# Kernel optimization log

Hardware: AMD Instinct MI355X
Metric: run time of the kernel (lower is better)

The kernel has to match this reference:

```python
import jax, jax.numpy as jnp
import numpy as np

DIM = 512
HIDDEN = DIM * 4


def _act_quant(x):
    # per-token int8 absmax quant over last axis (BitNet b1.58)
    scale = 127.0 / jnp.clip(jnp.max(jnp.abs(x), axis=-1, keepdims=True), 1e-5)
    return jnp.clip(jnp.round(x * scale), -128.0, 127.0) / scale


def _weight_quant(w):
    # ternary {-1,0,1} quant with global mean-abs scale
    scale = 1.0 / jnp.clip(jnp.mean(jnp.abs(w)), 1e-5)
    return jnp.clip(jnp.round(w * scale), -1.0, 1.0) / scale


def _bitlinear(x, w, b):
    # straight-through estimator: forward uses quantized values
    xq = x + jax.lax.stop_gradient(_act_quant(x) - x)
    wq = w + jax.lax.stop_gradient(_weight_quant(w) - w)
    return jnp.einsum('btd,hd->bth', xq, wq) + b


def setup_inputs() -> dict:
    key = jax.random.key(0)
    k1, k2, k3 = jax.random.split(key, 3)
    x = jax.random.normal(k1, (8, 8192, DIM), dtype=jnp.float32)
    w1 = jax.random.normal(k2, (HIDDEN, DIM), dtype=jnp.float32) * (DIM ** -0.5)
    b1 = jnp.zeros((HIDDEN,), dtype=jnp.float32)
    w2 = jax.random.normal(k3, (DIM, HIDDEN), dtype=jnp.float32) * (HIDDEN ** -0.5)
    b2 = jnp.zeros((DIM,), dtype=jnp.float32)
    return {"x": x, "w1": w1, "b1": b1, "w2": w2, "b2": b2}


def reference(x, w1, b1, w2, b2):
    h = _bitlinear(x, w1, b1)                      # [B,T,HIDDEN]
    h = jax.nn.gelu(h, approximate=False)          # exact erf GELU (nn.GELU default)
    return x + _bitlinear(h, w2, b2)               # residual
```

## Files before the change

### kernel.cpp

```cpp
#include <hip/hip_runtime.h>
#include <hip/hip_bf16.h>

#define DIM 512
#define HID 2048
#define MT  64
#define KS1 8
#define KS2 32

typedef __attribute__((ext_vector_type(4))) int      i32x4;
typedef __attribute__((ext_vector_type(4))) unsigned u32x4;

static __device__ __forceinline__ float gelu_erf(float h) {
  const float u  = h * 0.70710678118654752f;
  const float au = fabsf(u);
  const float t  = __builtin_amdgcn_rcpf(fmaf(0.3275911f, au, 1.f));
  float p = fmaf(1.061405429f, t, -1.453152027f);
  p = fmaf(p, t, 1.421413741f);
  p = fmaf(p, t, -0.284496736f);
  p = fmaf(p, t, 0.254829592f);
  p *= t;
  const float e  = __builtin_amdgcn_exp2f(-u * u * 1.4426950408889634f);
  const float ea = fmaf(-p, e, 1.f);
  const float er = __builtin_copysignf(ea, u);
  return fmaf(0.5f * h, er, 0.5f * h);
}

static __device__ __forceinline__ int qi8(float g, float s) {
  return (int)fminf(fmaxf(rintf(g * s), -128.f), 127.f);
}

static __device__ __forceinline__ unsigned q4pack(float4 v, float scl) {
  int q0 = qi8(v.x, scl), q1 = qi8(v.y, scl), q2 = qi8(v.z, scl), q3 = qi8(v.w, scl);
  return (unsigned)(q0 & 255) | ((unsigned)(q1 & 255) << 8) |
         ((unsigned)(q2 & 255) << 16) | ((unsigned)(q3 & 255) << 24);
}

__global__ void k_wabs(const float* __restrict__ w1, const float* __restrict__ w2,
                       float* __restrict__ part) {
  const int b = blockIdx.x;
  const float* src = (b < 256 ? w1 : w2) + (size_t)(b & 255) * 4096 + threadIdx.x * 16;
  float s = 0.f;
#pragma unroll
  for (int i = 0; i < 4; ++i) {
    float4 v = *(const float4*)(src + i * 4);
    s += fabsf(v.x) + fabsf(v.y) + fabsf(v.z) + fabsf(v.w);
  }
  __shared__ float red[256];
  red[threadIdx.x] = s;
  __syncthreads();
  for (int off = 128; off > 0; off >>= 1) {
    if (threadIdx.x < (unsigned)off) red[threadIdx.x] += red[threadIdx.x + off];
    __syncthreads();
  }
  if (threadIdx.x == 0) part[b] = red[0];
}

__global__ void k_wscale(const float* __restrict__ part, float* __restrict__ scales) {
  __shared__ float s1[256], s2[256];
  s1[threadIdx.x] = part[threadIdx.x];
  s2[threadIdx.x] = part[256 + threadIdx.x];
  __syncthreads();
  for (int off = 128; off > 0; off >>= 1) {
    if (threadIdx.x < (unsigned)off) {
      s1[threadIdx.x] += s1[threadIdx.x + off];
      s2[threadIdx.x] += s2[threadIdx.x + off];
    }
    __syncthreads();
  }
  if (threadIdx.x == 0) {
    const float mc1 = fmaxf(s1[0] / 1048576.f, 1e-5f);
    const float mc2 = fmaxf(s2[0] / 1048576.f, 1e-5f);
    scales[0] = mc1; scales[1] = 1.f / mc1;
    scales[2] = mc2; scales[3] = 1.f / mc2;
  }
}

__global__ void k_pack(const float* __restrict__ w1, const float* __restrict__ w2,
                       const float* __restrict__ scales,
                       signed char* __restrict__ p1, signed char* __restrict__ p2) {
  int slot = blockIdx.x * 256 + threadIdx.x;
  const bool isw2 = slot >= 65536;
  const float* w = isw2 ? w2 : w1;
  const float scl = isw2 ? scales[3] : scales[1];
  signed char* p = isw2 ? p2 : p1;
  const int K  = isw2 ? HID : DIM;
  const int KS = isw2 ? KS2 : KS1;
  slot &= 65535;
  const int lane = slot & 63;
  const int fr   = slot >> 6;
  const int nt   = fr / KS;
  const int ks   = fr - nt * KS;
  const int n  = nt * 16 + (lane & 15);
  const int k0 = ks * 64 + (lane >> 4) * 16;
  const float* src = w + (size_t)n * K + k0;
  i32x4 outv;
#pragma unroll
  for (int d = 0; d < 4; ++d) {
    unsigned v = 0;
#pragma unroll
    for (int e = 0; e < 4; ++e) {
      int q = (int)fminf(fmaxf(rintf(src[d * 4 + e] * scl), -1.f), 1.f);
      v |= ((unsigned)(q & 255)) << (8 * e);
    }
    outv[d] = (int)v;
  }
  *(i32x4*)(p + (size_t)slot * 16) = outv;
}

__global__ __launch_bounds__(1024, 4) void k_fused(
    const float* __restrict__ x, const float* __restrict__ b1,
    const float* __restrict__ b2, const signed char* __restrict__ p1,
    const signed char* __restrict__ p2, const float* __restrict__ scales,
    float* __restrict__ out) {
  __shared__ __align__(16) signed char qh[131072];
  __shared__ __align__(16) signed char xq[32768];

  float* rxTab = (float*)qh;
  float* scrP  = (float*)(qh + 1024);
  float* scrQ  = (float*)(qh + 5120);
  float* scrS  = (float*)(qh + 9216);

  const int tid = threadIdx.x;
  const int wv = tid >> 6, ln = tid & 63, lg = ln >> 4, lr = ln & 15;
  const int tok0 = blockIdx.x * MT;
  const float wsc1 = scales[0], wsc2 = scales[2];
  const int swz = (lr & 7) << 4;

  {
    const int row = tid >> 4, sub = tid & 15;
    const float4* xr = (const float4*)(x + (size_t)(tok0 + row) * DIM);
    float4 v[8];
    float am = 0.f;
#pragma unroll
    for (int i = 0; i < 8; ++i) {
      v[i] = xr[i * 16 + sub];
      am = fmaxf(am, fmaxf(fmaxf(fabsf(v[i].x), fabsf(v[i].y)),
                           fmaxf(fabsf(v[i].z), fabsf(v[i].w))));
    }
#pragma unroll
    for (int m = 1; m < 16; m <<= 1) am = fmaxf(am, __shfl_xor(am, m));
    const float mc  = fmaxf(am, 1e-5f);
    const float scl = 127.f / mc;
    if (sub == 0) rxTab[row] = mc * (1.f / 127.f) * wsc1;
    const int rswz = (row & 7) << 4;
#pragma unroll
    for (int i = 0; i < 8; ++i) {
      const unsigned u = q4pack(v[i], scl);
      const int k = i * 64 + sub * 4;
      *(unsigned*)&xq[row * DIM + (((k & ~15) ^ rswz) | (k & 15))] = u;
    }
  }
  __syncthreads();

  float rxw[4];
#pragma unroll
  for (int mt = 0; mt < 4; ++mt) rxw[mt] = rxTab[mt * 16 + lr];

  float hvmax[4], hvmin[4];
#pragma unroll
  for (int mt = 0; mt < 4; ++mt) { hvmax[mt] = -3.4e38f; hvmin[mt] = 3.4e38f; }

#pragma unroll 1
  for (int ch = 0; ch < 4; ++ch) {
    i32x4 acc[2][4];
#pragma unroll
    for (int t = 0; t < 2; ++t)
#pragma unroll
      for (int mt = 0; mt < 4; ++mt) acc[t][mt] = (i32x4){0, 0, 0, 0};
#pragma unroll 2
    for (int ks = 0; ks < KS1; ++ks) {
      i32x4 a[4];
#pragma unroll
      for (int mt = 0; mt < 4; ++mt)
        a[mt] = *(const i32x4*)&xq[(mt * 16 + lr) * DIM + ((ks * 64 + lg * 16) ^ swz)];
#pragma unroll
      for (int t = 0; t < 2; ++t) {
        const int ntg = wv * 8 + ch * 2 + t;
        const i32x4 bfr = *(const i32x4*)(p1 + ((size_t)(ntg * KS1 + ks) * 64 + ln) * 16);
#pragma unroll
        for (int mt = 0; mt < 4; ++mt)
          acc[t][mt] = __builtin_amdgcn_mfma_i32_16x16x64_i8(bfr, a[mt], acc[t][mt], 0, 0, 0);
      }
    }
#pragma unroll
    for (int t = 0; t < 2; ++t) {
      const int ntg = wv * 8 + ch * 2 + t;
      const float4 b4 = *(const float4*)&b1[ntg * 16 + lg * 4];
#pragma unroll
      for (int mt = 0; mt < 4; ++mt) {
#pragma unroll
        for (int r = 0; r < 4; ++r) {
          const float bias = r == 0 ? b4.x : r == 1 ? b4.y : r == 2 ? b4.z : b4.w;
          const float hv = fmaf((float)acc[t][mt][r], rxw[mt], bias);
          hvmax[mt] = fmaxf(hvmax[mt], hv);
          hvmin[mt] = fminf(hvmin[mt], hv);
        }
      }
    }
  }

#pragma unroll
  for (int mt = 0; mt < 4; ++mt) {
    hvmax[mt] = fmaxf(hvmax[mt], __shfl_xor(hvmax[mt], 16));
    hvmax[mt] = fmaxf(hvmax[mt], __shfl_xor(hvmax[mt], 32));
    hvmin[mt] = fminf(hvmin[mt], __shfl_xor(hvmin[mt], 16));
    hvmin[mt] = fminf(hvmin[mt], __shfl_xor(hvmin[mt], 32));
  }
  if (ln < 16) {
#pragma unroll
    for (int mt = 0; mt < 4; ++mt) {
      scrP[wv * 64 + mt * 16 + lr] = hvmax[mt];
      scrQ[wv * 64 + mt * 16 + lr] = hvmin[mt];
    }
  }
  __syncthreads();
  if (tid < MT) {
    float hx = scrP[tid], hn = scrQ[tid];
#pragma unroll
    for (int w = 1; w < 16; ++w) {
      hx = fmaxf(hx, scrP[w * 64 + tid]);
      hn = fminf(hn, scrQ[w * 64 + tid]);
    }
    const float posg = gelu_erf(hx);
    const float negg = (hn <= -0.7518f) ? 0.1699705f : fabsf(gelu_erf(hn));
    const float mg = fmaxf(fmaxf(posg, negg), 1e-5f);
    scrS[tid] = 127.f / mg;
  }
  __syncthreads();

  float s2w[4];
#pragma unroll
  for (int mt = 0; mt < 4; ++mt) s2w[mt] = scrS[mt * 16 + lr];
  __syncthreads();

#pragma unroll 1
  for (int ch = 0; ch < 4; ++ch) {
    i32x4 acc[2][4];
#pragma unroll
    for (int t = 0; t < 2; ++t)
#pragma unroll
      for (int mt = 0; mt < 4; ++mt) acc[t][mt] = (i32x4){0, 0, 0, 0};
#pragma unroll 2
    for (int ks = 0; ks < KS1; ++ks) {
      i32x4 a[4];
#pragma unroll
      for (int mt = 0; mt < 4; ++mt)
        a[mt] = *(const i32x4*)&xq[(mt * 16 + lr) * DIM + ((ks * 64 + lg * 16) ^ swz)];
#pragma unroll
      for (int t = 0; t < 2; ++t) {
        const int ntg = wv * 8 + ch * 2 + t;
        const i32x4 bfr = *(const i32x4*)(p1 + ((size_t)(ntg * KS1 + ks) * 64 + ln) * 16);
#pragma unroll
        for (int mt = 0; mt < 4; ++mt)
          acc[t][mt] = __builtin_amdgcn_mfma_i32_16x16x64_i8(bfr, a[mt], acc[t][mt], 0, 0, 0);
      }
    }
#pragma unroll
    for (int t = 0; t < 2; ++t) {
      const int ntg = wv * 8 + ch * 2 + t;
      const float4 b4 = *(const float4*)&b1[ntg * 16 + lg * 4];
#pragma unroll
      for (int mt = 0; mt < 4; ++mt) {
        const int m = mt * 16 + lr;
        unsigned pk = 0;
#pragma unroll
        for (int r = 0; r < 4; ++r) {
          const float bias = r == 0 ? b4.x : r == 1 ? b4.y : r == 2 ? b4.z : b4.w;
          const float hv = fmaf((float)acc[t][mt][r], rxw[mt], bias);
          const float g  = gelu_erf(hv);
          pk |= ((unsigned)(qi8(g, s2w[mt]) & 255)) << (8 * r);
        }
        *(unsigned*)&qh[m * HID + (((ntg * 16) ^ ((m & 7) << 4)) + lg * 4)] = pk;
      }
    }
  }
  __syncthreads();

  i32x4 acc2[2][4];
#pragma unroll
  for (int t = 0; t < 2; ++t)
#pragma unroll
    for (int mt = 0; mt < 4; ++mt) acc2[t][mt] = (i32x4){0, 0, 0, 0};
#pragma unroll 2
  for (int ks = 0; ks < KS2; ++ks) {
    i32x4 a[4];
#pragma unroll
    for (int mt = 0; mt < 4; ++mt)
      a[mt] = *(const i32x4*)&qh[(mt * 16 + lr) * HID + ((ks * 64 + lg * 16) ^ swz)];
#pragma unroll
    for (int t = 0; t < 2; ++t) {
      const int nt = wv * 2 + t;
      const i32x4 bfr = *(const i32x4*)(p2 + ((size_t)(nt * KS2 + ks) * 64 + ln) * 16);
#pragma unroll
      for (int mt = 0; mt < 4; ++mt)
        acc2[t][mt] = __builtin_amdgcn_mfma_i32_16x16x64_i8(bfr, a[mt], acc2[t][mt], 0, 0, 0);
    }
  }
#pragma unroll
  for (int t = 0; t < 2; ++t) {
    const int n0 = (wv * 2 + t) * 16 + lg * 4;
    const float4 b4 = *(const float4*)&b2[n0];
#pragma unroll
    for (int mt = 0; mt < 4; ++mt) {
      const int m = mt * 16 + lr;
      const float r2 = wsc2 * __builtin_amdgcn_rcpf(s2w[mt]);
      const size_t gbase = (size_t)(tok0 + m) * DIM + n0;
      const float4 x4 = *(const float4*)&x[gbase];
      float4 o;
      o.x = fmaf((float)acc2[t][mt][0], r2, b4.x + x4.x);
      o.y = fmaf((float)acc2[t][mt][1], r2, b4.y + x4.y);
      o.z = fmaf((float)acc2[t][mt][2], r2, b4.z + x4.z);
      o.w = fmaf((float)acc2[t][mt][3], r2, b4.w + x4.w);
      *(float4*)&out[gbase] = o;
    }
  }
}

extern "C" void kernel_launch(void* const* d_in, const int* in_sizes, int n_in,
                              void* d_out, int out_size, void* d_ws, size_t ws_size,
                              hipStream_t stream) {
  const float* x  = (const float*)d_in[0];
  const float* w1 = (const float*)d_in[1];
  const float* b1 = (const float*)d_in[2];
  const float* w2 = (const float*)d_in[3];
  const float* b2 = (const float*)d_in[4];
  float* out = (float*)d_out;

  float* wpart   = (float*)d_ws;
  float* wscales = wpart + 512;
  signed char* p1 = (signed char*)((char*)d_ws + 4096);
  signed char* p2 = (signed char*)((char*)d_ws + 4096 + 1048576);

  k_wabs<<<512, 256, 0, stream>>>(w1, w2, wpart);
  k_wscale<<<1, 256, 0, stream>>>(wpart, wscales);
  k_pack<<<512, 256, 0, stream>>>(w1, w2, wscales, p1, p2);
  k_fused<<<1024, 1024, 0, stream>>>(x, b1, b2, p1, p2, wscales, out);
}
```

Baseline: 291.7 us.

## Compute first GEMM once, cache GELU outputs as fp16 in registers

Removes the second pass of the first int8 GEMM by computing GELU once, taking the exact per-token absmax, and holding the GELU values as packed fp16 in registers until the quantization scale is known. Token tile per block is halved to 32, shrinking shared memory and doubling the grid so more blocks can be resident. The trade-off is more register pressure, halved reuse of weight fragments per block, and fp16 round-toward-zero storage that can occasionally shift an int8 rounding decision.

```diff
diff --git a/kernel.cpp b/kernel.cpp
--- a/kernel.cpp
+++ b/kernel.cpp
@@ -3,12 +3,13 @@
 
 #define DIM 512
 #define HID 2048
-#define MT  64
+#define MT  32
 #define KS1 8
 #define KS2 32
 
 typedef __attribute__((ext_vector_type(4))) int      i32x4;
 typedef __attribute__((ext_vector_type(4))) unsigned u32x4;
+typedef __attribute__((ext_vector_type(2))) __fp16   fp16x2;
 
 static __device__ __forceinline__ float gelu_erf(float h) {
   const float u  = h * 0.70710678118654752f;
@@ -33,6 +34,16 @@
   int q0 = qi8(v.x, scl), q1 = qi8(v.y, scl), q2 = qi8(v.z, scl), q3 = qi8(v.w, scl);
   return (unsigned)(q0 & 255) | ((unsigned)(q1 & 255) << 8) |
          ((unsigned)(q2 & 255) << 16) | ((unsigned)(q3 & 255) << 24);
+}
+
+static __device__ __forceinline__ unsigned packf16(float a, float b) {
+  fp16x2 v = __builtin_amdgcn_cvt_pkrtz(a, b);
+  unsigned u; __builtin_memcpy(&u, &v, 4); return u;
+}
+static __device__ __forceinline__ float unpackf16(unsigned u, int hi) {
+  unsigned short s = (unsigned short)(hi ? (u >> 16) : (u & 0xffff));
+  __fp16 h; __builtin_memcpy(&h, &s, 2);
+  return (float)h;
 }
 
 __global__ void k_wabs(const float* __restrict__ w1, const float* __restrict__ w2,
@@ -112,13 +123,12 @@
     const float* __restrict__ b2, const signed char* __restrict__ p1,
     const signed char* __restrict__ p2, const float* __restrict__ scales,
     float* __restrict__ out) {
-  __shared__ __align__(16) signed char qh[131072];
-  __shared__ __align__(16) signed char xq[32768];
+  __shared__ __align__(16) signed char qh[MT * HID];
+  __shared__ __align__(16) signed char xq[MT * DIM];
 
   float* rxTab = (float*)qh;
   float* scrP  = (float*)(qh + 1024);
-  float* scrQ  = (float*)(qh + 5120);
-  float* scrS  = (float*)(qh + 9216);
+  float* scrS  = (float*)(qh + 4096);
 
   const int tid = threadIdx.x;
   const int wv = tid >> 6, ln = tid & 63, lg = ln >> 4, lr = ln & 15;
@@ -127,172 +137,152 @@
   const int swz = (lr & 7) << 4;
 
   {
-    const int row = tid >> 4, sub = tid & 15;
+    const int row = tid >> 5, sub = tid & 31;
     const float4* xr = (const float4*)(x + (size_t)(tok0 + row) * DIM);
-    float4 v[8];
+    float4 v[4];
     float am = 0.f;
 #pragma unroll
-    for (int i = 0; i < 8; ++i) {
-      v[i] = xr[i * 16 + sub];
+    for (int i = 0; i < 4; ++i) {
+      v[i] = xr[i * 32 + sub];
       am = fmaxf(am, fmaxf(fmaxf(fabsf(v[i].x), fabsf(v[i].y)),
                            fmaxf(fabsf(v[i].z), fabsf(v[i].w))));
     }
 #pragma unroll
-    for (int m = 1; m < 16; m <<= 1) am = fmaxf(am, __shfl_xor(am, m));
+    for (int m = 1; m < 32; m <<= 1) am = fmaxf(am, __shfl_xor(am, m));
     const float mc  = fmaxf(am, 1e-5f);
     const float scl = 127.f / mc;
     if (sub == 0) rxTab[row] = mc * (1.f / 127.f) * wsc1;
     const int rswz = (row & 7) << 4;
 #pragma unroll
-    for (int i = 0; i < 8; ++i) {
+    for (int i = 0; i < 4; ++i) {
       const unsigned u = q4pack(v[i], scl);
-      const int k = i * 64 + sub * 4;
-      *(unsigned*)&xq[row * DIM + (((k & ~15) ^ rswz) | (k & 15))] = u;
-    }
-  }
-  __syncthreads();
-
-  float rxw[4];
-#pragma unroll
-  for (int mt = 0; mt < 4; ++mt) rxw[mt] = rxTab[mt * 16 + lr];
-
-  float hvmax[4], hvmin[4];
-#pragma unroll
-  for (int mt = 0; mt < 4; ++mt) { hvmax[mt] = -3.4e38f; hvmin[mt] = 3.4e38f; }
-
-#pragma unroll 1
-  for (int ch = 0; ch < 4; ++ch) {
-    i32x4 acc[2][4];
-#pragma unroll
-    for (int t = 0; t < 2; ++t)
-#pragma unroll
-      for (int mt = 0; mt < 4; ++mt) acc[t][mt] = (i32x4){0, 0, 0, 0};
-#pragma unroll 2
-    for (int ks = 0; ks < KS1; ++ks) {
-      i32x4 a[4];
-#pragma unroll
-      for (int mt = 0; mt < 4; ++mt)
-        a[mt] = *(const i32x4*)&xq[(mt * 16 + lr) * DIM + ((ks * 64 + lg * 16) ^ swz)];
-#pragma unroll
-      for (int t = 0; t < 2; ++t) {
-        const int ntg = wv * 8 + ch * 2 + t;
-        const i32x4 bfr = *(const i32x4*)(p1 + ((size_t)(ntg * KS1 + ks) * 64 + ln) * 16);
-#pragma unroll
-        for (int mt = 0; mt < 4; ++mt)
-          acc[t][mt] = __builtin_amdgcn_mfma_i32_16x16x64_i8(bfr, a[mt], acc[t][mt], 0, 0, 0);
-      }
-    }
+      const int c = (i * 32 + sub) * 4;
+      *(unsigned*)&xq[row * DIM + (((c & ~15) ^ rswz) | (c & 15))] = u;
+    }
+  }
+  __syncthreads();
+
+  float rxw[2];
+#pragma unroll
+  for (int mt = 0; mt < 2; ++mt) rxw[mt] = rxTab[mt * 16 + lr];
+
+  unsigned gpk[4][2][2][2];
+  float gmax[2] = {0.f, 0.f};
+
+#define G1CHUNK(CH)                                                               \
+  {                                                                               \
+    i32x4 acc[2][2];                                                              \
+    _Pragma("unroll")                                                             \
+    for (int t = 0; t < 2; ++t)                                                   \
+      _Pragma("unroll")                                                           \
+      for (int mt = 0; mt < 2; ++mt) acc[t][mt] = (i32x4){0, 0, 0, 0};            \
+    _Pragma("unroll 2")                                                           \
+    for (int ks = 0; ks < KS1; ++ks) {                                            \
+      i32x4 a[2];                                                                 \
+      _Pragma("unroll")                                                           \
+      for (int mt = 0; mt < 2; ++mt)                                              \
+        a[mt] = *(const i32x4*)&xq[(mt * 16 + lr) * DIM +                         \
+                                   ((ks * 64 + lg * 16) ^ swz)];                  \
+      _Pragma("unroll")                                                           \
+      for (int t = 0; t < 2; ++t) {                                               \
+        const int ntg = wv * 8 + (CH) * 2 + t;                                    \
+        const i32x4 bfr =                                                         \
+            *(const i32x4*)(p1 + ((size_t)(ntg * KS1 + ks) * 64 + ln) * 16);      \
+        _Pragma("unroll")                                                         \
+        for (int mt = 0; mt < 2; ++mt)                                            \
+          acc[t][mt] =                                                            \
+              __builtin_amdgcn_mfma_i32_16x16x64_i8(bfr, a[mt], acc[t][mt],       \
+                                                    0, 0, 0);                     \
+      }                                                                           \
+    }                                                                             \
+    _Pragma("unroll")                                                             \
+    for (int t = 0; t < 2; ++t) {                                                 \
+      const int ntg = wv * 8 + (CH) * 2 + t;                                      \
+      const float4 b4 = *(const float4*)&b1[ntg * 16 + lg * 4];                   \
+      _Pragma("unroll")                                                           \
+      for (int mt = 0; mt < 2; ++mt) {                                            \
+        float gv[4];                                                              \
+        _Pragma("unroll")                                                         \
+        for (int r = 0; r < 4; ++r) {                                             \
+          const float bias = r == 0 ? b4.x : r == 1 ? b4.y : r == 2 ? b4.z        \
+                                                                    : b4.w;       \
+          const float hv = fmaf((float)acc[t][mt][r], rxw[mt], bias);             \
+          gv[r] = gelu_erf(hv);                                                   \
+          gmax[mt] = fmaxf(gmax[mt], fabsf(gv[r]));                               \
+        }                                                                         \
+        gpk[CH][t][mt][0] = packf16(gv[0], gv[1]);                                \
+        gpk[CH][t][mt][1] = packf16(gv[2], gv[3]);                                \
+      }                                                                           \
+    }                                                                             \
+  }
+
+  G1CHUNK(0)
+  G1CHUNK(1)
+  G1CHUNK(2)
+  G1CHUNK(3)
+#undef G1CHUNK
+
+#pragma unroll
+  for (int mt = 0; mt < 2; ++mt) {
+    gmax[mt] = fmaxf(gmax[mt], __shfl_xor(gmax[mt], 16));
+    gmax[mt] = fmaxf(gmax[mt], __shfl_xor(gmax[mt], 32));
+  }
+  if (ln < 16) {
+#pragma unroll
+    for (int mt = 0; mt < 2; ++mt) scrP[wv * 32 + mt * 16 + lr] = gmax[mt];
+  }
+  __syncthreads();
+  if (tid < MT) {
+    float mg = scrP[tid];
+#pragma unroll
+    for (int w = 1; w < 16; ++w) mg = fmaxf(mg, scrP[w * 32 + tid]);
+    scrS[tid] = 127.f / fmaxf(mg, 1e-5f);
+  }
+  __syncthreads();
+  float s2w[2];
+#pragma unroll
+  for (int mt = 0; mt < 2; ++mt) s2w[mt] = scrS[mt * 16 + lr];
+  __syncthreads();
+
+#pragma unroll
+  for (int ch = 0; ch < 4; ++ch)
 #pragma unroll
     for (int t = 0; t < 2; ++t) {
       const int ntg = wv * 8 + ch * 2 + t;
-      const float4 b4 = *(const float4*)&b1[ntg * 16 + lg * 4];
-#pragma unroll
-      for (int mt = 0; mt < 4; ++mt) {
-#pragma unroll
-        for (int r = 0; r < 4; ++r) {
-          const float bias = r == 0 ? b4.x : r == 1 ? b4.y : r == 2 ? b4.z : b4.w;
-          const float hv = fmaf((float)acc[t][mt][r], rxw[mt], bias);
-          hvmax[mt] = fmaxf(hvmax[mt], hv);
-          hvmin[mt] = fminf(hvmin[mt], hv);
-        }
-      }
-    }
-  }
-
-#pragma unroll
-  for (int mt = 0; mt < 4; ++mt) {
-    hvmax[mt] = fmaxf(hvmax[mt], __shfl_xor(hvmax[mt], 16));
-    hvmax[mt] = fmaxf(hvmax[mt], __shfl_xor(hvmax[mt], 32));
-    hvmin[mt] = fminf(hvmin[mt], __shfl_xor(hvmin[mt], 16));
-    hvmin[mt] = fminf(hvmin[mt], __shfl_xor(hvmin[mt], 32));
-  }
-  if (ln < 16) {
-#pragma unroll
-    for (int mt = 0; mt < 4; ++mt) {
-      scrP[wv * 64 + mt * 16 + lr] = hvmax[mt];
-      scrQ[wv * 64 + mt * 16 + lr] = hvmin[mt];
-    }
-  }
-  __syncthreads();
-  if (tid < MT) {
-    float hx = scrP[tid], hn = scrQ[tid];
-#pragma unroll
-    for (int w = 1; w < 16; ++w) {
-      hx = fmaxf(hx, scrP[w * 64 + tid]);
-      hn = fminf(hn, scrQ[w * 64 + tid]);
-    }
-    const float posg = gelu_erf(hx);
-    const float negg = (hn <= -0.7518f) ? 0.1699705f : fabsf(gelu_erf(hn));
-    const float mg = fmaxf(fmaxf(posg, negg), 1e-5f);
-    scrS[tid] = 127.f / mg;
-  }
-  __syncthreads();
-
-  float s2w[4];
-#pragma unroll
-  for (int mt = 0; mt < 4; ++mt) s2w[mt] = scrS[mt * 16 + lr];
-  __syncthreads();
-
-#pragma unroll 1
-  for (int ch = 0; ch < 4; ++ch) {
-    i32x4 acc[2][4];
-#pragma unroll
-    for (int t = 0; t < 2; ++t)
-#pragma unroll
-      for (int mt = 0; mt < 4; ++mt) acc[t][mt] = (i32x4){0, 0, 0, 0};
-#pragma unroll 2
-    for (int ks = 0; ks < KS1; ++ks) {
-      i32x4 a[4];
-#pragma unroll
-      for (int mt = 0; mt < 4; ++mt)
-        a[mt] = *(const i32x4*)&xq[(mt * 16 + lr) * DIM + ((ks * 64 + lg * 16) ^ swz)];
-#pragma unroll
-      for (int t = 0; t < 2; ++t) {
-        const int ntg = wv * 8 + ch * 2 + t;
-        const i32x4 bfr = *(const i32x4*)(p1 + ((size_t)(ntg * KS1 + ks) * 64 + ln) * 16);
-#pragma unroll
-        for (int mt = 0; mt < 4; ++mt)
-          acc[t][mt] = __builtin_amdgcn_mfma_i32_16x16x64_i8(bfr, a[mt], acc[t][mt], 0, 0, 0);
-      }
-    }
-#pragma unroll
-    for (int t = 0; t < 2; ++t) {
-      const int ntg = wv * 8 + ch * 2 + t;
-      const float4 b4 = *(const float4*)&b1[ntg * 16 + lg * 4];
-#pragma unroll
-      for (int mt = 0; mt < 4; ++mt) {
+#pragma unroll
+      for (int mt = 0; mt < 2; ++mt) {
         const int m = mt * 16 + lr;
         unsigned pk = 0;
 #pragma unroll
-        for (int r = 0; r < 4; ++r) {
-          const float bias = r == 0 ? b4.x : r == 1 ? b4.y : r == 2 ? b4.z : b4.w;
-          const float hv = fmaf((float)acc[t][mt][r], rxw[mt], bias);
-          const float g  = gelu_erf(hv);
-          pk |= ((unsigned)(qi8(g, s2w[mt]) & 255)) << (8 * r);
+        for (int pr = 0; pr < 2; ++pr) {
+          const unsigned v = gpk[ch][t][mt][pr];
+          const int q0 = qi8(unpackf16(v, 0), s2w[mt]);
+          const int q1 = qi8(unpackf16(v, 1), s2w[mt]);
+          pk |= ((unsigned)(q0 & 255)) << (16 * pr);
+          pk |= ((unsigned)(q1 & 255)) << (16 * pr + 8);
         }
         *(unsigned*)&qh[m * HID + (((ntg * 16) ^ ((m & 7) << 4)) + lg * 4)] = pk;
       }
     }
-  }
-  __syncthreads();
-
-  i32x4 acc2[2][4];
+  __syncthreads();
+
+  i32x4 acc2[2][2];
 #pragma unroll
   for (int t = 0; t < 2; ++t)
 #pragma unroll
-    for (int mt = 0; mt < 4; ++mt) acc2[t][mt] = (i32x4){0, 0, 0, 0};
+    for (int mt = 0; mt < 2; ++mt) acc2[t][mt] = (i32x4){0, 0, 0, 0};
 #pragma unroll 2
   for (int ks = 0; ks < KS2; ++ks) {
-    i32x4 a[4];
-#pragma unroll
-    for (int mt = 0; mt < 4; ++mt)
+    i32x4 a[2];
+#pragma unroll
+    for (int mt = 0; mt < 2; ++mt)
       a[mt] = *(const i32x4*)&qh[(mt * 16 + lr) * HID + ((ks * 64 + lg * 16) ^ swz)];
 #pragma unroll
     for (int t = 0; t < 2; ++t) {
       const int nt = wv * 2 + t;
       const i32x4 bfr = *(const i32x4*)(p2 + ((size_t)(nt * KS2 + ks) * 64 + ln) * 16);
 #pragma unroll
-      for (int mt = 0; mt < 4; ++mt)
+      for (int mt = 0; mt < 2; ++mt)
         acc2[t][mt] = __builtin_amdgcn_mfma_i32_16x16x64_i8(bfr, a[mt], acc2[t][mt], 0, 0, 0);
     }
   }
@@ -301,7 +291,7 @@
     const int n0 = (wv * 2 + t) * 16 + lg * 4;
     const float4 b4 = *(const float4*)&b2[n0];
 #pragma unroll
-    for (int mt = 0; mt < 4; ++mt) {
+    for (int mt = 0; mt < 2; ++mt) {
       const int m = mt * 16 + lr;
       const float r2 = wsc2 * __builtin_amdgcn_rcpf(s2w[mt]);
       const size_t gbase = (size_t)(tok0 + m) * DIM + n0;
@@ -334,5 +324,5 @@
   k_wabs<<<512, 256, 0, stream>>>(w1, w2, wpart);
   k_wscale<<<1, 256, 0, stream>>>(wpart, wscales);
   k_pack<<<512, 256, 0, stream>>>(w1, w2, wscales, p1, p2);
-  k_fused<<<1024, 1024, 0, stream>>>(x, b1, b2, p1, p2, wscales, out);
-}
+  k_fused<<<2048, 1024, 0, stream>>>(x, b1, b2, p1, p2, wscales, out);
+}
```

After: 330.9 us. +13.4%, slower.
